# Kernel optimization log

Measured on AMD Instinct MI355X. Metric: run time of the kernel, lower is better.

Reference implementation:

```python
import jax, jax.numpy as jnp
import numpy as np

NUM_ENTS = 100000
NUM_RELS2 = 460  # num_rels * 2
H = 128
T = 4            # sequence_len snapshots
E = 200000       # edges per snapshot
SLOPE = (1.0 / 8.0 + 1.0 / 3.0) / 2.0  # F.rrelu in eval mode -> leaky with mean slope


def l2norm(x):
    # torch F.normalize(dim=1)
    n = jnp.linalg.norm(x, axis=-1, keepdims=True)
    return x / jnp.maximum(n, 1e-12)


def gru_cell(x, h, Wx, Wh, bx, bh):
    # torch.nn.GRUCell math
    gx = x @ Wx.T + bx  # [*, 3H]
    gh = h @ Wh.T + bh
    xr, xz, xn = jnp.split(gx, 3, axis=-1)
    hr, hz, hn = jnp.split(gh, 3, axis=-1)
    r = jax.nn.sigmoid(xr + hr)
    z = jax.nn.sigmoid(xz + hz)
    n = jnp.tanh(xn + r * hn)
    return (1.0 - z) * n + z * h


def rgcn_layer(h, rel, src, dst, etype, Wn, Wl):
    # UnionRGCNLayer (convgcn): msg = (h[src] + rel_emb[etype]) @ W_neighbor,
    # sum-aggregate to dst, normalize by in-degree, add self-loop transform, rrelu.
    msg = (h[src] + rel[etype]) @ Wn                        # [E, H]
    agg = jax.ops.segment_sum(msg, dst, num_segments=NUM_ENTS)
    deg = jax.ops.segment_sum(jnp.ones((msg.shape[0],), msg.dtype), dst,
                              num_segments=NUM_ENTS)
    agg = agg / jnp.maximum(deg, 1.0)[:, None]
    out = agg + h @ Wl                                      # self-loop
    return jnp.where(out >= 0, out, SLOPE * out)


def setup_inputs() -> dict:
    key = jax.random.key(0)
    ks = jax.random.split(key, 24)
    s = 0.05
    inp = {
        'src': jax.random.randint(ks[0], (T, E), 0, NUM_ENTS),
        'dst': jax.random.randint(ks[1], (T, E), 0, NUM_ENTS),
        'etype': jax.random.randint(ks[2], (T, E), 0, NUM_RELS2),
        'dynamic_emb': jax.random.normal(ks[3], (NUM_ENTS, H), jnp.float32),
        'emb_rel': jax.random.normal(ks[4], (NUM_RELS2, H), jnp.float32) * s,
        'Wn1': jax.random.normal(ks[5], (H, H), jnp.float32) * s,
        'Wl1': jax.random.normal(ks[6], (H, H), jnp.float32) * s,
        'Wn2': jax.random.normal(ks[7], (H, H), jnp.float32) * s,
        'Wl2': jax.random.normal(ks[8], (H, H), jnp.float32) * s,
        'gru_r_Wx': jax.random.normal(ks[9], (3 * H, 2 * H), jnp.float32) * s,
        'gru_r_Wh': jax.random.normal(ks[10], (3 * H, H), jnp.float32) * s,
        'gru_r_bx': jnp.zeros((3 * H,), jnp.float32),
        'gru_r_bh': jnp.zeros((3 * H,), jnp.float32),
        'gate_W': jax.random.normal(ks[11], (H, 2 * H), jnp.float32) * s,
        'gate_b': jnp.zeros((H,), jnp.float32),
        'tdiff_W': jax.random.normal(ks[12], (H, H), jnp.float32) * s,
        'tdiff_b': jnp.zeros((H,), jnp.float32),
        'time_gate_W': jax.random.normal(ks[13], (H, H), jnp.float32) * s,
        'time_gate_b': jnp.zeros((H,), jnp.float32),
    }
    return inp


def reference(src, dst, etype, dynamic_emb, emb_rel, Wn1, Wl1, Wn2, Wl2,
              gru_r_Wx, gru_r_Wh, gru_r_bx, gru_r_bh,
              gate_W, gate_b, tdiff_W, tdiff_b, time_gate_W, time_gate_b):
    h0 = l2norm(dynamic_emb)  # layer_norm=True path (F.normalize)

    def step(carry, g):
        h, rel = carry
        s, d, et = g
        # relation evolution via GRUCell(2H -> H)
        x_in = jnp.concatenate([emb_rel, rel], axis=1)
        rel_new = gru_cell(x_in, rel, gru_r_Wx, gru_r_Wh, gru_r_bx, gru_r_bh)
        # 2-layer RGCN message passing on snapshot graph
        cur = rgcn_layer(h, rel_new, s, d, et, Wn1, Wl1)
        cur = rgcn_layer(cur, rel_new, s, d, et, Wn2, Wl2)
        cur = l2norm(cur)
        # time gate
        tw = jax.nn.sigmoid(cur @ time_gate_W + time_gate_b)
        h_new = tw * cur + (1.0 - tw) * h
        # GatedFusion(current, prev)
        gate = jax.nn.sigmoid(jnp.concatenate([h_new, h], axis=1) @ gate_W.T + gate_b)
        h_new = gate * h_new + (1.0 - gate) * h
        # TemporalDifferenceFusion(current, prev)
        h_new = h_new + jax.nn.relu((h_new - h) @ tdiff_W.T + tdiff_b)
        return (h_new, rel_new), None

    (h, rel), _ = jax.lax.scan(step, (h0, emb_rel), (src, dst, etype))
    return h
```

## Files before the change

### kernel.cpp

```cpp
#include <hip/hip_runtime.h>
#include <hip/hip_bf16.h>

#define N_ENT 100000
#define HDIM 128
#define NE 200000
#define NR 460
#define NSTEP 4
#define SLOPE 0.22916666666666666f
#define NPAD 100352
#define SCAN_NB 98
#define HGRID 782

typedef __attribute__((ext_vector_type(8))) short short8;
typedef __attribute__((ext_vector_type(4))) float f32x4;

__device__ __forceinline__ float sigm(float x) { return 1.0f / (1.0f + __expf(-x)); }
__device__ __forceinline__ short f2bs(float f) {
    __hip_bfloat16 b = __float2bfloat16(f);
    short s; __builtin_memcpy(&s, &b, 2); return s;
}
__device__ __forceinline__ float bs2f(short s) {
    union { unsigned int u; float f; } c;
    c.u = ((unsigned int)(unsigned short)s) << 16;
    return c.f;
}

__global__ void zero_int_kernel(int* __restrict__ p, int n)
{
    int i = blockIdx.x * 256 + threadIdx.x;
    if (i < n) p[i] = 0;
}

__global__ void diag_kernel(float* o, float v)
{
    if (threadIdx.x == 0) o[0] = v;
}

__global__ __launch_bounds__(256)
void hist_gru_kernel(const int* __restrict__ dst, int* __restrict__ cnt,
                     float* rel, short* __restrict__ relb,
                     const float* __restrict__ emb_rel,
                     const float* __restrict__ WxT, const float* __restrict__ WhT,
                     const float* __restrict__ bx, const float* __restrict__ bh)
{
    if (blockIdx.x < HGRID) {
        int e = blockIdx.x * 256 + threadIdx.x;
        if (e < NE) atomicAdd(&cnt[dst[e]], 1);
        return;
    }
    __shared__ __align__(16) float x[256];
    __shared__ __align__(16) float hh[128];
    int b = blockIdx.x - HGRID;
    int j = threadIdx.x;
    float hj = 0.0f;
    if (j < 128) {
        hj = rel[b * HDIM + j];
        x[j] = emb_rel[b * HDIM + j];
        x[128 + j] = hj;
        hh[j] = hj;
    }
    __syncthreads();
    if (j >= 128) return;
    float xr = 0, xz = 0, xn = 0, hr = 0, hz = 0, hn = 0;
    for (int k = 0; k < 256; k++) {
        float xv = x[k];
        const float* w = &WxT[k * 384];
        xr += xv * w[j]; xz += xv * w[128 + j]; xn += xv * w[256 + j];
    }
    for (int k = 0; k < 128; k++) {
        float hv = hh[k];
        const float* w = &WhT[k * 384];
        hr += hv * w[j]; hz += hv * w[128 + j]; hn += hv * w[256 + j];
    }
    float r = sigm(xr + bx[j] + hr + bh[j]);
    float z = sigm(xz + bx[128 + j] + hz + bh[128 + j]);
    float n = tanhf(xn + bx[256 + j] + r * (hn + bh[256 + j]));
    float nv = (1.0f - z) * n + z * hj;
    rel[b * HDIM + j] = nv;
    relb[b * HDIM + j] = f2bs(nv);
}

__global__ __launch_bounds__(256)
void scan1_kernel(const int* __restrict__ cnt, int* __restrict__ rowptr,
                  int* __restrict__ bsum)
{
    __shared__ int ts[256];
    int b = blockIdx.x, t = threadIdx.x;
    int base = b * 1024 + t * 4;
    int4 v = *(const int4*)&cnt[base];
    int s = v.x + v.y + v.z + v.w;
    ts[t] = s;
    __syncthreads();
    for (int off = 1; off < 256; off <<= 1) {
        int x = 0;
        if (t >= off) x = ts[t - off];
        __syncthreads();
        if (t >= off) ts[t] += x;
        __syncthreads();
    }
    int excl = ts[t] - s;
    if (t == 255) bsum[b] = ts[t];
    rowptr[base + 0] = excl;
    rowptr[base + 1] = excl + v.x;
    rowptr[base + 2] = excl + v.x + v.y;
    rowptr[base + 3] = excl + v.x + v.y + v.z;
}

__global__ __launch_bounds__(128)
void scan2_kernel(int* __restrict__ bsum, int nb)
{
    __shared__ int ts[128];
    int t = threadIdx.x;
    int v = (t < nb) ? bsum[t] : 0;
    ts[t] = v;
    __syncthreads();
    for (int off = 1; off < 128; off <<= 1) {
        int x = 0;
        if (t >= off) x = ts[t - off];
        __syncthreads();
        if (t >= off) ts[t] += x;
        __syncthreads();
    }
    if (t < nb) bsum[t] = ts[t] - v;
}

__global__ void fill_kernel(const int* __restrict__ dst,
                            const int* __restrict__ rowptr,
                            const int* __restrict__ bsum,
                            int* __restrict__ cnt, int* __restrict__ eidx)
{
    int e = blockIdx.x * 256 + threadIdx.x;
    if (e < NE) {
        int d = dst[e];
        int p = atomicAdd(&cnt[d], -1);
        eidx[rowptr[d] + bsum[d >> 10] + p - 1] = e;
    }
}

__global__ void prep_kernel(
    const float* __restrict__ emb_rel,
    const float* __restrict__ Wx, const float* __restrict__ Wh,
    const float* __restrict__ Wn1, const float* __restrict__ Wl1,
    const float* __restrict__ Wn2, const float* __restrict__ Wl2,
    const float* __restrict__ tgW, const float* __restrict__ gateW,
    const float* __restrict__ tdW,
    float* __restrict__ rel,
    float* __restrict__ WxT, float* __restrict__ WhT,
    short* __restrict__ BT1, short* __restrict__ BT2,
    short* __restrict__ BTe1, short* __restrict__ BTe2,
    short* __restrict__ BTe3)
{
    int tid = blockIdx.x * blockDim.x + threadIdx.x;
    int nthr = gridDim.x * blockDim.x;
    for (int i = tid; i < NR * HDIM; i += nthr)
        rel[i] = emb_rel[i];
    for (int i = tid; i < 384 * 256; i += nthr) {
        int r = i >> 8, c = i & 255;
        WxT[c * 384 + r] = Wx[i];
    }
    for (int i = tid; i < 384 * 128; i += nthr) {
        int r = i >> 7, c = i & 127;
        WhT[c * 384 + r] = Wh[i];
    }
    for (int i = tid; i < 128 * 256; i += nthr) {
        int n = i >> 8, k = i & 255;
        float v1 = (k < 128) ? Wn1[k * 128 + n] : Wl1[(k - 128) * 128 + n];
        float v2 = (k < 128) ? Wn2[k * 128 + n] : Wl2[(k - 128) * 128 + n];
        BT1[n * 256 + k] = f2bs(v1);
        BT2[n * 256 + k] = f2bs(v2);
    }
    for (int i = tid; i < 128 * 128; i += nthr) {
        int n = i >> 7, k = i & 127;
        BTe1[n * 128 + k] = f2bs(tgW[k * 128 + n]);
        BTe3[n * 128 + k] = f2bs(tdW[n * 128 + k]);
    }
    for (int i = tid; i < 128 * 256; i += nthr) {
        int n = i >> 8, k = i & 255;
        BTe2[n * 256 + k] = f2bs(gateW[n * 256 + k]);
    }
}

__global__ __launch_bounds__(64)
void norm_init_kernel(const float* __restrict__ emb, short* __restrict__ hb)
{
    int row = blockIdx.x, lane = threadIdx.x;
    float v0 = emb[row * HDIM + lane];
    float v1 = emb[row * HDIM + 64 + lane];
    float s = v0 * v0 + v1 * v1;
    #pragma unroll
    for (int off = 32; off; off >>= 1) s += __shfl_xor(s, off);
    float invn = 1.0f / fmaxf(sqrtf(s), 1e-12f);
    hb[row * HDIM + lane] = f2bs(v0 * invn);
    hb[row * HDIM + 64 + lane] = f2bs(v1 * invn);
}

__global__ __launch_bounds__(256)
void gather_kernel(const int* __restrict__ src, const int* __restrict__ et,
                   const int* __restrict__ eidx, const int* __restrict__ rowptr,
                   const int* __restrict__ bsum,
                   const short* __restrict__ hb, const short* __restrict__ relb,
                   short* __restrict__ aggb, int lo, int hi)
{
    int idx = blockIdx.x * 256 + threadIdx.x;
    int r = lo + (idx >> 3);
    if (r >= hi) return;
    int c16 = (idx & 7) * 16;
    int p0 = rowptr[r] + bsum[r >> 10];
    int p1 = rowptr[r + 1] + bsum[(r + 1) >> 10];
    float v[16];
    #pragma unroll
    for (int j = 0; j < 16; j++) v[j] = 0.0f;

    int p = p0;
    for (; p + 2 <= p1; p += 2) {
        int e0 = eidx[p], e1 = eidx[p + 1];
        int s0 = src[e0], t0 = et[e0];
        int s1 = src[e1], t1 = et[e1];
        short8 h00 = *(const short8*)&hb[(long)s0 * HDIM + c16];
        short8 h01 = *(const short8*)&hb[(long)s0 * HDIM + c16 + 8];
        short8 h10 = *(const short8*)&hb[(long)s1 * HDIM + c16];
        short8 h11 = *(const short8*)&hb[(long)s1 * HDIM + c16 + 8];
        short8 r00 = *(const short8*)&relb[t0 * HDIM + c16];
        short8 r01 = *(const short8*)&relb[t0 * HDIM + c16 + 8];
        short8 r10 = *(const short8*)&relb[t1 * HDIM + c16];
        short8 r11 = *(const short8*)&relb[t1 * HDIM + c16 + 8];
        #pragma unroll
        for (int j = 0; j < 8; j++) {
            v[j]     += bs2f(h00[j]) + bs2f(r00[j]) + bs2f(h10[j]) + bs2f(r10[j]);
            v[8 + j] += bs2f(h01[j]) + bs2f(r01[j]) + bs2f(h11[j]) + bs2f(r11[j]);
        }
    }
    if (p < p1) {
        int e0 = eidx[p];
        int s0 = src[e0], t0 = et[e0];
        short8 h00 = *(const short8*)&hb[(long)s0 * HDIM + c16];
        short8 h01 = *(const short8*)&hb[(long)s0 * HDIM + c16 + 8];
        short8 r00 = *(const short8*)&relb[t0 * HDIM + c16];
        short8 r01 = *(const short8*)&relb[t0 * HDIM + c16 + 8];
        #pragma unroll
        for (int j = 0; j < 8; j++) {
            v[j]     += bs2f(h00[j]) + bs2f(r00[j]);
            v[8 + j] += bs2f(h01[j]) + bs2f(r01[j]);
        }
    }

    float rdeg = (p1 > p0) ? 1.0f / (float)(p1 - p0) : 0.0f;
    short8 o0, o1;
    #pragma unroll
    for (int j = 0; j < 8; j++) {
        o0[j] = f2bs(v[j] * rdeg);
        o1[j] = f2bs(v[8 + j] * rdeg);
    }
    *(short8*)&aggb[(long)(r - lo) * HDIM + c16] = o0;
    *(short8*)&aggb[(long)(r - lo) * HDIM + c16 + 8] = o1;
}

template<int F32OUT>
__global__ __launch_bounds__(256, 2)
void layer_gemm(const short* __restrict__ aggb, const short* __restrict__ hb,
                const short* __restrict__ BTg, float* __restrict__ outf,
                short* __restrict__ outb, int lo, int hi)
{
    __shared__ __align__(16) short smBT[128 * 256];
    const int tid = threadIdx.x;

    #pragma unroll
    for (int it = 0; it < 16; it++) {
        int s = it * 256 + tid;
        int row = s >> 5, k8 = s & 31;
        short8 v = *(const short8*)&BTg[row * 256 + k8 * 8];
        *(short8*)&smBT[row * 256 + 8 * (k8 ^ (row & 7))] = v;
    }
    __syncthreads();

    const int lane = tid & 63;
    const int wv = tid >> 6;
    const int m = lane & 15, q = lane >> 4;
    const int rowBase = lo + blockIdx.x * 256 + wv * 64;

    f32x4 acc[4][8];
    #pragma unroll
    for (int rt = 0; rt < 4; rt++)
        #pragma unroll
        for (int ct = 0; ct < 8; ct++)
            acc[rt][ct] = (f32x4)0.0f;

    for (int kc = 0; kc < 8; kc++) {
        short8 a[4];
        #pragma unroll
        for (int rt = 0; rt < 4; rt++) {
            int row = rowBase + rt * 16 + m;
            int k0 = kc * 32 + q * 8;
            if (row < hi) {
                if (kc < 4) {
                    a[rt] = *(const short8*)&aggb[(long)(row - lo) * HDIM + k0];
                } else {
                    a[rt] = *(const short8*)&hb[(long)row * HDIM + (k0 - 128)];
                }
            } else {
                short8 t;
                #pragma unroll
                for (int i = 0; i < 8; i++) t[i] = 0;
                a[rt] = t;
            }
        }
        short8 b[8];
        #pragma unroll
        for (int ct = 0; ct < 8; ct++)
            b[ct] = *(const short8*)&smBT[(ct * 16 + m) * 256
                                          + 8 * ((kc * 4 + q) ^ (m & 7))];
        #pragma unroll
        for (int rt = 0; rt < 4; rt++)
            #pragma unroll
            for (int ct = 0; ct < 8; ct++)
                acc[rt][ct] = __builtin_amdgcn_mfma_f32_16x16x32_bf16(
                    a[rt], b[ct], acc[rt][ct], 0, 0, 0);
    }

    #pragma unroll
    for (int rt = 0; rt < 4; rt++) {
        #pragma unroll
        for (int rg = 0; rg < 4; rg++) {
            int row = rowBase + rt * 16 + q * 4 + rg;
            if (row >= hi) continue;
            #pragma unroll
            for (int ct = 0; ct < 8; ct++) {
                int col = ct * 16 + m;
                float c = acc[rt][ct][rg];
                c = c >= 0.0f ? c : SLOPE * c;
                if (F32OUT) outf[(long)row * HDIM + col] = c;
                else        outb[(long)row * HDIM + col] = f2bs(c);
            }
        }
    }
}

#define ER 32
#define ES 136

__device__ __forceinline__ void stage_tile(
    const float* __restrict__ curf, const short* __restrict__ curb,
    const short* __restrict__ hb, long rb, int tid, int wf,
    short* cs, short* hd)
{
    #pragma unroll
    for (int it = 0; it < 2; it++) {
        int s = it * 256 + tid;
        int r = s >> 4, c8 = (s & 15) * 8;
        float x[8];
        if (wf) {
            const float* pc = &curf[(rb + r) * HDIM + c8];
            float4 c0 = *(const float4*)pc, c1 = *(const float4*)(pc + 4);
            x[0]=c0.x; x[1]=c0.y; x[2]=c0.z; x[3]=c0.w;
            x[4]=c1.x; x[5]=c1.y; x[6]=c1.z; x[7]=c1.w;
        } else {
            short8 cv = *(const short8*)&curb[(rb + r) * HDIM + c8];
            #pragma unroll
            for (int j = 0; j < 8; j++) x[j] = bs2f(cv[j]);
        }
        short8 th = *(const short8*)&hb[(rb + r) * HDIM + c8];
        float ss = x[0]*x[0] + x[1]*x[1] + x[2]*x[2] + x[3]*x[3]
                 + x[4]*x[4] + x[5]*x[5] + x[6]*x[6] + x[7]*x[7];
        ss += __shfl_xor(ss, 1);
        ss += __shfl_xor(ss, 2);
        ss += __shfl_xor(ss, 4);
        ss += __shfl_xor(ss, 8);
        float inv = 1.0f / fmaxf(sqrtf(ss), 1e-12f);
        short8 tc;
        #pragma unroll
        for (int j = 0; j < 8; j++) tc[j] = f2bs(x[j] * inv);
        *(short8*)&cs[r * ES + c8] = tc;
        *(short8*)&hd[r * ES + c8] = th;
    }
}

__device__ __forceinline__ void mm128_d(const short* As0, const short* As1,
                                        const short* __restrict__ Bg,
                                        int wr0, int ct0, int m, int q,
                                        f32x4 a0[4], f32x4 a1[4])
{
    #pragma unroll
    for (int ct = 0; ct < 4; ct++) { a0[ct] = (f32x4)0.0f; a1[ct] = (f32x4)0.0f; }
    #pragma unroll
    for (int kc = 0; kc < 4; kc++) {
        int k0 = kc * 32 + q * 8;
        short8 av0 = *(const short8*)&As0[(wr0 + m) * ES + k0];
        short8 av1 = *(const short8*)&As1[(wr0 + m) * ES + k0];
        #pragma unroll
        for (int ct = 0; ct < 4; ct++) {
            short8 b = *(const short8*)&Bg[((ct0 + ct) * 16 + m) * 128 + k0];
            a0[ct] = __builtin_amdgcn_mfma_f32_16x16x32_bf16(av0, b, a0[ct], 0, 0, 0);
            a1[ct] = __builtin_amdgcn_mfma_f32_16x16x32_bf16(av1, b, a1[ct], 0, 0, 0);
        }
    }
}

__device__ __forceinline__ void mm256_d(const short* cs0, const short* hd0,
                                        const short* cs1, const short* hd1,
                                        const short* __restrict__ Bg,
                                        int wr0, int ct0, int m, int q,
                                        f32x4 a0[4], f32x4 a1[4])
{
    #pragma unroll
    for (int ct = 0; ct < 4; ct++) { a0[ct] = (f32x4)0.0f; a1[ct] = (f32x4)0.0f; }
    #pragma unroll
    for (int kc = 0; kc < 8; kc++) {
        int k0 = kc * 32 + q * 8;
        short8 av0 = (kc < 4) ? *(const short8*)&cs0[(wr0 + m) * ES + k0]
                              : *(const short8*)&hd0[(wr0 + m) * ES + (k0 - 128)];
        short8 av1 = (kc < 4) ? *(const short8*)&cs1[(wr0 + m) * ES + k0]
                              : *(const short8*)&hd1[(wr0 + m) * ES + (k0 - 128)];
        #pragma unroll
        for (int ct = 0; ct < 4; ct++) {
            short8 b = *(const short8*)&Bg[((ct0 + ct) * 16 + m) * 256 + k0];
            a0[ct] = __builtin_amdgcn_mfma_f32_16x16x32_bf16(av0, b, a0[ct], 0, 0, 0);
            a1[ct] = __builtin_amdgcn_mfma_f32_16x16x32_bf16(av1, b, a1[ct], 0, 0, 0);
        }
    }
}

__device__ __forceinline__ void epi1_f(const f32x4 acc[4], const float btr[4],
                                       short* cs, const short* hd,
                                       int wr0, int ct0, int m, int q)
{
    #pragma unroll
    for (int ct = 0; ct < 4; ct++) {
        int col = (ct0 + ct) * 16 + m;
        #pragma unroll
        for (int rg = 0; rg < 4; rg++) {
            int rl = wr0 + q * 4 + rg;
            float tw = sigm(acc[ct][rg] + btr[ct]);
            float curn = bs2f(cs[rl * ES + col]);
            float hv = bs2f(hd[rl * ES + col]);
            cs[rl * ES + col] = f2bs(tw * curn + (1.0f - tw) * hv);
        }
    }
}

__device__ __forceinline__ void epi2_f(const f32x4 acc[4], const float bgr[4],
                                       short* cs, short* hd,
                                       int wr0, int ct0, int m, int q)
{
    #pragma unroll
    for (int ct = 0; ct < 4; ct++) {
        int col = (ct0 + ct) * 16 + m;
        #pragma unroll
        for (int rg = 0; rg < 4; rg++) {
            int rl = wr0 + q * 4 + rg;
            float g = sigm(acc[ct][rg] + bgr[ct]);
            float h1v = bs2f(cs[rl * ES + col]);
            float hv = bs2f(hd[rl * ES + col]);
            float h2 = g * h1v + (1.0f - g) * hv;
            cs[rl * ES + col] = f2bs(h2);
            hd[rl * ES + col] = f2bs(h2 - hv);
        }
    }
}

__device__ __forceinline__ void fin_f(const f32x4 acc[4], const float btdr[4],
                                      short* cs, long rb,
                                      float* __restrict__ outp, int wf,
                                      int wr0, int ct0, int m, int q)
{
    #pragma unroll
    for (int ct = 0; ct < 4; ct++) {
        int col = (ct0 + ct) * 16 + m;
        #pragma unroll
        for (int rg = 0; rg < 4; rg++) {
            int rl = wr0 + q * 4 + rg;
            float td = fmaxf(acc[ct][rg] + btdr[ct], 0.0f);
            float val = bs2f(cs[rl * ES + col]) + td;
            if (wf) outp[(rb + rl) * HDIM + col] = val;
            else    cs[rl * ES + col] = f2bs(val);
        }
    }
}

__global__ __launch_bounds__(256, 4)
void fused_epi_kernel(const float* __restrict__ curf, const short* __restrict__ curb,
                      const short* __restrict__ hb,
                      const short* __restrict__ BTe1, const short* __restrict__ BTe2,
                      const short* __restrict__ BTe3,
                      const float* __restrict__ bt, const float* __restrict__ bg,
                      const float* __restrict__ btd,
                      float* __restrict__ outp, short* __restrict__ abfo, int wf)
{
    __shared__ __align__(16) short cs[2][ER * ES];
    __shared__ __align__(16) short hd[2][ER * ES];
    const int tid = threadIdx.x;
    const long row0 = (long)blockIdx.x * (2 * ER);
    const long row1 = row0 + ER;
    const bool t1v = (row1 < N_ENT);

    stage_tile(curf, curb, hb, row0, tid, wf, cs[0], hd[0]);
    if (t1v) stage_tile(curf, curb, hb, row1, tid, wf, cs[1], hd[1]);
    __syncthreads();

    const int wv = tid >> 6, lane = tid & 63;
    const int m = lane & 15, q = lane >> 4;
    const int wr0 = (wv >> 1) * 16;
    const int ct0 = (wv & 1) * 4;

    float btr[4], bgr[4], btdr[4];
    #pragma unroll
    for (int ct = 0; ct < 4; ct++) {
        btr[ct]  = bt[(ct0 + ct) * 16 + m];
        bgr[ct]  = bg[(ct0 + ct) * 16 + m];
        btdr[ct] = btd[(ct0 + ct) * 16 + m];
    }

    f32x4 a0[4], a1[4];

    mm128_d(cs[0], cs[1], BTe1, wr0, ct0, m, q, a0, a1);
    __syncthreads();
    epi1_f(a0, btr, cs[0], hd[0], wr0, ct0, m, q);
    epi1_f(a1, btr, cs[1], hd[1], wr0, ct0, m, q);
    __syncthreads();

    mm256_d(cs[0], hd[0], cs[1], hd[1], BTe2, wr0, ct0, m, q, a0, a1);
    __syncthreads();
    epi2_f(a0, bgr, cs[0], hd[0], wr0, ct0, m, q);
    epi2_f(a1, bgr, cs[1], hd[1], wr0, ct0, m, q);
    __syncthreads();

    mm128_d(hd[0], hd[1], BTe3, wr0, ct0, m, q, a0, a1);
    fin_f(a0, btdr, cs[0], row0, outp, wf, wr0, ct0, m, q);
    if (t1v) fin_f(a1, btdr, cs[1], row1, outp, wf, wr0, ct0, m, q);

    if (!wf) {
        __syncthreads();
        #pragma unroll
        for (int it = 0; it < 4; it++) {
            int slot = it * 256 + tid;
            int tile = slot >> 9;
            int rr = (slot >> 4) & 31;
            int c8 = (slot & 15) * 8;
            if (tile == 0 || t1v) {
                long gr = row0 + tile * ER + rr;
                *(short8*)&abfo[gr * HDIM + c8] =
                    *(const short8*)&cs[tile][rr * ES + c8];
            }
        }
    }
}

extern "C" void kernel_launch(void* const* d_in, const int* in_sizes, int n_in,
                              void* d_out, int out_size, void* d_ws, size_t ws_size,
                              hipStream_t stream)
{
    const int* src = (const int*)d_in[0];
    const int* dst = (const int*)d_in[1];
    const int* ety = (const int*)d_in[2];
    const float* dyn     = (const float*)d_in[3];
    const float* emb_rel = (const float*)d_in[4];
    const float* Wn1     = (const float*)d_in[5];
    const float* Wl1     = (const float*)d_in[6];
    const float* Wn2     = (const float*)d_in[7];
    const float* Wl2     = (const float*)d_in[8];
    const float* gWx     = (const float*)d_in[9];
    const float* gWh     = (const float*)d_in[10];
    const float* gbx     = (const float*)d_in[11];
    const float* gbh     = (const float*)d_in[12];
    const float* gateW   = (const float*)d_in[13];
    const float* gateb   = (const float*)d_in[14];
    const float* tdW     = (const float*)d_in[15];
    const float* tdb     = (const float*)d_in[16];
    const float* tgW     = (const float*)d_in[17];
    const float* tgb     = (const float*)d_in[18];

    const long NH = (long)N_ENT * HDIM;
    float* ws = (float*)d_ws;
    long off = 0;
    short* Abf  = (short*)(ws + off); off += NH / 2;
    short* Bb   = (short*)(ws + off); off += NH / 2;
    short* Cb   = (short*)(ws + off); off += NH / 2;
    float* rel  = ws + off; off += (long)NR * HDIM;
    short* relb = (short*)(ws + off); off += (NR * HDIM) / 2;
    float* WxT  = ws + off; off += 98304;
    float* WhT  = ws + off; off += 49152;
    short* BT1  = (short*)(ws + off); off += 16384;
    short* BT2  = (short*)(ws + off); off += 16384;
    short* BTe1 = (short*)(ws + off); off += 8192;
    short* BTe2 = (short*)(ws + off); off += 16384;
    short* BTe3 = (short*)(ws + off); off += 8192;
    int* rowptr = (int*)(ws + off); off += NPAD;
    int* cnt    = (int*)(ws + off); off += NPAD;
    int* eidx   = (int*)(ws + off); off += 200704;
    int* bsum   = (int*)(ws + off); off += 128;
    short* aggb = (short*)(ws + off);
    float* C    = (float*)d_out;

    const long avail = (long)(ws_size / 4) - off;
    const int cand[5] = {100000, 50000, 25008, 12512, 6256};
    int chunk = -1;
    for (int c = 0; c < 5; c++)
        if (avail >= (long)cand[c] * 64) { chunk = cand[c]; break; }

    if (chunk < 0) {
        diag_kernel<<<1, 64, 0, stream>>>((float*)d_out, (float)ws_size);
        return;
    }

    prep_kernel<<<256, 256, 0, stream>>>(
        emb_rel, gWx, gWh, Wn1, Wl1, Wn2, Wl2, tgW, gateW, tdW,
        rel, WxT, WhT, BT1, BT2, BTe1, BTe2, BTe3);

    norm_init_kernel<<<N_ENT, 64, 0, stream>>>(dyn, Abf);

    zero_int_kernel<<<(NPAD + 255) / 256, 256, 0, stream>>>(cnt, NPAD);

    const int egrid = (NE + 255) / 256;
    const int fe_grid = (N_ENT + 63) / 64;

    for (int t = 0; t < NSTEP; t++) {
        const int* st = src + (long)t * NE;
        const int* dt = dst + (long)t * NE;
        const int* et = ety + (long)t * NE;

        hist_gru_kernel<<<HGRID + NR, 256, 0, stream>>>(
            dt, cnt, rel, relb, emb_rel, WxT, WhT, gbx, gbh);
        scan1_kernel<<<SCAN_NB, 256, 0, stream>>>(cnt, rowptr, bsum);
        scan2_kernel<<<1, 128, 0, stream>>>(bsum, SCAN_NB);
        fill_kernel<<<egrid, 256, 0, stream>>>(dt, rowptr, bsum, cnt, eidx);

        int wf = (t == NSTEP - 1) ? 1 : 0;

        for (int lo = 0; lo < N_ENT; lo += chunk) {
            int hi = lo + chunk > N_ENT ? N_ENT : lo + chunk;
            gather_kernel<<<((hi - lo) * 8 + 255) / 256, 256, 0, stream>>>(
                st, et, eidx, rowptr, bsum, Abf, relb, aggb, lo, hi);
            layer_gemm<0><<<(hi - lo + 255) / 256, 256, 0, stream>>>(
                aggb, Abf, BT1, nullptr, Bb, lo, hi);
        }
        for (int lo = 0; lo < N_ENT; lo += chunk) {
            int hi = lo + chunk > N_ENT ? N_ENT : lo + chunk;
            gather_kernel<<<((hi - lo) * 8 + 255) / 256, 256, 0, stream>>>(
                st, et, eidx, rowptr, bsum, Bb, relb, aggb, lo, hi);
            if (wf)
                layer_gemm<1><<<(hi - lo + 255) / 256, 256, 0, stream>>>(
                    aggb, Bb, BT2, C, nullptr, lo, hi);
            else
                layer_gemm<0><<<(hi - lo + 255) / 256, 256, 0, stream>>>(
                    aggb, Bb, BT2, nullptr, Cb, lo, hi);
        }

        fused_epi_kernel<<<fe_grid, 256, 0, stream>>>(
            C, Cb, Abf, BTe1, BTe2, BTe3, tgb, gateb, tdb, C, Abf, wf);
    }
}
```

Measured before the change: 908.6 us.

## Batch CSR build for all snapshots upfront and fold GRU into epilogue kernel

Builds the destination-sorted edge index (histogram, scan, fill) for all four snapshots at once using 2D grids before the time loop, instead of four per-step kernels inside it. The relation GRU for the next step is merged into the tail blocks of the fused epilogue kernel, with a standalone GRU kernel only for the first step. This cuts per-step launches and serial dependencies. The cost is four times the CSR workspace and extra branching in the epilogue kernel.

```diff
diff --git a/kernel.cpp b/kernel.cpp
--- a/kernel.cpp
+++ b/kernel.cpp
@@ -9,7 +9,9 @@
 #define SLOPE 0.22916666666666666f
 #define NPAD 100352
 #define SCAN_NB 98
-#define HGRID 782
+#define EGRID 782
+#define ESZ 200704
+#define FEG 1563
 
 typedef __attribute__((ext_vector_type(8))) short short8;
 typedef __attribute__((ext_vector_type(4))) float f32x4;
@@ -36,104 +38,71 @@
     if (threadIdx.x == 0) o[0] = v;
 }
 
+__global__ void hist4_kernel(const int* __restrict__ dst, int* __restrict__ cnt4)
+{
+    int t = blockIdx.y;
+    int e = blockIdx.x * 256 + threadIdx.x;
+    if (e < NE) atomicAdd(&cnt4[t * NPAD + dst[(long)t * NE + e]], 1);
+}
+
 __global__ __launch_bounds__(256)
-void hist_gru_kernel(const int* __restrict__ dst, int* __restrict__ cnt,
-                     float* rel, short* __restrict__ relb,
-                     const float* __restrict__ emb_rel,
-                     const float* __restrict__ WxT, const float* __restrict__ WhT,
-                     const float* __restrict__ bx, const float* __restrict__ bh)
-{
-    if (blockIdx.x < HGRID) {
-        int e = blockIdx.x * 256 + threadIdx.x;
-        if (e < NE) atomicAdd(&cnt[dst[e]], 1);
-        return;
-    }
-    __shared__ __align__(16) float x[256];
-    __shared__ __align__(16) float hh[128];
-    int b = blockIdx.x - HGRID;
-    int j = threadIdx.x;
-    float hj = 0.0f;
-    if (j < 128) {
-        hj = rel[b * HDIM + j];
-        x[j] = emb_rel[b * HDIM + j];
-        x[128 + j] = hj;
-        hh[j] = hj;
-    }
-    __syncthreads();
-    if (j >= 128) return;
-    float xr = 0, xz = 0, xn = 0, hr = 0, hz = 0, hn = 0;
-    for (int k = 0; k < 256; k++) {
-        float xv = x[k];
-        const float* w = &WxT[k * 384];
-        xr += xv * w[j]; xz += xv * w[128 + j]; xn += xv * w[256 + j];
-    }
-    for (int k = 0; k < 128; k++) {
-        float hv = hh[k];
-        const float* w = &WhT[k * 384];
-        hr += hv * w[j]; hz += hv * w[128 + j]; hn += hv * w[256 + j];
-    }
-    float r = sigm(xr + bx[j] + hr + bh[j]);
-    float z = sigm(xz + bx[128 + j] + hz + bh[128 + j]);
-    float n = tanhf(xn + bx[256 + j] + r * (hn + bh[256 + j]));
-    float nv = (1.0f - z) * n + z * hj;
-    rel[b * HDIM + j] = nv;
-    relb[b * HDIM + j] = f2bs(nv);
-}
-
-__global__ __launch_bounds__(256)
-void scan1_kernel(const int* __restrict__ cnt, int* __restrict__ rowptr,
-                  int* __restrict__ bsum)
+void scan1_4_kernel(const int* __restrict__ cnt4, int* __restrict__ rowptr4,
+                    int* __restrict__ bsum4)
 {
     __shared__ int ts[256];
-    int b = blockIdx.x, t = threadIdx.x;
-    int base = b * 1024 + t * 4;
-    int4 v = *(const int4*)&cnt[base];
+    int t = blockIdx.y;
+    int b = blockIdx.x, tt = threadIdx.x;
+    int base = t * NPAD + b * 1024 + tt * 4;
+    int4 v = *(const int4*)&cnt4[base];
     int s = v.x + v.y + v.z + v.w;
-    ts[t] = s;
+    ts[tt] = s;
     __syncthreads();
     for (int off = 1; off < 256; off <<= 1) {
         int x = 0;
-        if (t >= off) x = ts[t - off];
+        if (tt >= off) x = ts[tt - off];
         __syncthreads();
-        if (t >= off) ts[t] += x;
+        if (tt >= off) ts[tt] += x;
         __syncthreads();
     }
-    int excl = ts[t] - s;
-    if (t == 255) bsum[b] = ts[t];
-    rowptr[base + 0] = excl;
-    rowptr[base + 1] = excl + v.x;
-    rowptr[base + 2] = excl + v.x + v.y;
-    rowptr[base + 3] = excl + v.x + v.y + v.z;
+    int excl = ts[tt] - s;
+    if (tt == 255) bsum4[t * 128 + b] = ts[tt];
+    rowptr4[base + 0] = excl;
+    rowptr4[base + 1] = excl + v.x;
+    rowptr4[base + 2] = excl + v.x + v.y;
+    rowptr4[base + 3] = excl + v.x + v.y + v.z;
 }
 
 __global__ __launch_bounds__(128)
-void scan2_kernel(int* __restrict__ bsum, int nb)
+void scan2_4_kernel(int* __restrict__ bsum4)
 {
     __shared__ int ts[128];
-    int t = threadIdx.x;
-    int v = (t < nb) ? bsum[t] : 0;
-    ts[t] = v;
+    int t = blockIdx.x;
+    int tt = threadIdx.x;
+    int v = (tt < SCAN_NB) ? bsum4[t * 128 + tt] : 0;
+    ts[tt] = v;
     __syncthreads();
     for (int off = 1; off < 128; off <<= 1) {
         int x = 0;
-        if (t >= off) x = ts[t - off];
+        if (tt >= off) x = ts[tt - off];
         __syncthreads();
-        if (t >= off) ts[t] += x;
+        if (tt >= off) ts[tt] += x;
         __syncthreads();
     }
-    if (t < nb) bsum[t] = ts[t] - v;
-}
-
-__global__ void fill_kernel(const int* __restrict__ dst,
-                            const int* __restrict__ rowptr,
-                            const int* __restrict__ bsum,
-                            int* __restrict__ cnt, int* __restrict__ eidx)
-{
+    if (tt < SCAN_NB) bsum4[t * 128 + tt] = ts[tt] - v;
+}
+
+__global__ void fill4_kernel(const int* __restrict__ dst,
+                             const int* __restrict__ rowptr4,
+                             const int* __restrict__ bsum4,
+                             int* __restrict__ cnt4, int* __restrict__ eidx4)
+{
+    int t = blockIdx.y;
     int e = blockIdx.x * 256 + threadIdx.x;
     if (e < NE) {
-        int d = dst[e];
-        int p = atomicAdd(&cnt[d], -1);
-        eidx[rowptr[d] + bsum[d >> 10] + p - 1] = e;
+        int d = dst[(long)t * NE + e];
+        int p = atomicAdd(&cnt4[t * NPAD + d], -1);
+        eidx4[(long)t * ESZ + rowptr4[t * NPAD + d]
+              + bsum4[t * 128 + (d >> 10)] + p - 1] = e;
     }
 }
 
@@ -192,6 +161,39 @@
     float invn = 1.0f / fmaxf(sqrtf(s), 1e-12f);
     hb[row * HDIM + lane] = f2bs(v0 * invn);
     hb[row * HDIM + 64 + lane] = f2bs(v1 * invn);
+}
+
+__global__ __launch_bounds__(128)
+void gru_kernel(float* rel, short* __restrict__ relb,
+                const float* __restrict__ emb_rel,
+                const float* __restrict__ WxT, const float* __restrict__ WhT,
+                const float* __restrict__ bx, const float* __restrict__ bh)
+{
+    __shared__ __align__(16) float x[256];
+    __shared__ __align__(16) float hh[128];
+    int b = blockIdx.x, j = threadIdx.x;
+    float hj = rel[b * HDIM + j];
+    x[j] = emb_rel[b * HDIM + j];
+    x[128 + j] = hj;
+    hh[j] = hj;
+    __syncthreads();
+    float xr = 0, xz = 0, xn = 0, hr = 0, hz = 0, hn = 0;
+    for (int k = 0; k < 256; k++) {
+        float xv = x[k];
+        const float* w = &WxT[k * 384];
+        xr += xv * w[j]; xz += xv * w[128 + j]; xn += xv * w[256 + j];
+    }
+    for (int k = 0; k < 128; k++) {
+        float hv = hh[k];
+        const float* w = &WhT[k * 384];
+        hr += hv * w[j]; hz += hv * w[128 + j]; hn += hv * w[256 + j];
+    }
+    float r = sigm(xr + bx[j] + hr + bh[j]);
+    float z = sigm(xz + bx[128 + j] + hz + bh[128 + j]);
+    float n = tanhf(xn + bx[256 + j] + r * (hn + bh[256 + j]));
+    float nv = (1.0f - z) * n + z * hj;
+    rel[b * HDIM + j] = nv;
+    relb[b * HDIM + j] = f2bs(nv);
 }
 
 __global__ __launch_bounds__(256)
@@ -483,11 +485,50 @@
                       const short* __restrict__ BTe3,
                       const float* __restrict__ bt, const float* __restrict__ bg,
                       const float* __restrict__ btd,
-                      float* __restrict__ outp, short* __restrict__ abfo, int wf)
+                      float* __restrict__ outp, short* __restrict__ abfo, int wf,
+                      float* rel, short* __restrict__ relb,
+                      const float* __restrict__ emb_rel,
+                      const float* __restrict__ WxT, const float* __restrict__ WhT,
+                      const float* __restrict__ gbx, const float* __restrict__ gbh)
 {
     __shared__ __align__(16) short cs[2][ER * ES];
     __shared__ __align__(16) short hd[2][ER * ES];
     const int tid = threadIdx.x;
+
+    if (blockIdx.x >= FEG) {
+        float* x = (float*)cs;
+        float* hh = x + 256;
+        int b = blockIdx.x - FEG;
+        int j = tid;
+        float hj = 0.0f;
+        if (j < 128) {
+            hj = rel[b * HDIM + j];
+            x[j] = emb_rel[b * HDIM + j];
+            x[128 + j] = hj;
+            hh[j] = hj;
+        }
+        __syncthreads();
+        if (j >= 128) return;
+        float xr = 0, xz = 0, xn = 0, hr = 0, hz = 0, hn = 0;
+        for (int k = 0; k < 256; k++) {
+            float xv = x[k];
+            const float* w = &WxT[k * 384];
+            xr += xv * w[j]; xz += xv * w[128 + j]; xn += xv * w[256 + j];
+        }
+        for (int k = 0; k < 128; k++) {
+            float hv = hh[k];
+            const float* w = &WhT[k * 384];
+            hr += hv * w[j]; hz += hv * w[128 + j]; hn += hv * w[256 + j];
+        }
+        float r = sigm(xr + gbx[j] + hr + gbh[j]);
+        float z = sigm(xz + gbx[128 + j] + hz + gbh[128 + j]);
+        float n = tanhf(xn + gbx[256 + j] + r * (hn + gbh[256 + j]));
+        float nv = (1.0f - z) * n + z * hj;
+        rel[b * HDIM + j] = nv;
+        relb[b * HDIM + j] = f2bs(nv);
+        return;
+    }
+
     const long row0 = (long)blockIdx.x * (2 * ER);
     const long row1 = row0 + ER;
     const bool t1v = (row1 < N_ENT);
@@ -583,10 +624,10 @@
     short* BTe1 = (short*)(ws + off); off += 8192;
     short* BTe2 = (short*)(ws + off); off += 16384;
     short* BTe3 = (short*)(ws + off); off += 8192;
-    int* rowptr = (int*)(ws + off); off += NPAD;
-    int* cnt    = (int*)(ws + off); off += NPAD;
-    int* eidx   = (int*)(ws + off); off += 200704;
-    int* bsum   = (int*)(ws + off); off += 128;
+    int* rowptr4 = (int*)(ws + off); off += 4 * NPAD;
+    int* cnt4    = (int*)(ws + off); off += 4 * NPAD;
+    int* eidx4   = (int*)(ws + off); off += 4 * ESZ;
+    int* bsum4   = (int*)(ws + off); off += 4 * 128;
     short* aggb = (short*)(ws + off);
     float* C    = (float*)d_out;
 
@@ -607,35 +648,37 @@
 
     norm_init_kernel<<<N_ENT, 64, 0, stream>>>(dyn, Abf);
 
-    zero_int_kernel<<<(NPAD + 255) / 256, 256, 0, stream>>>(cnt, NPAD);
-
-    const int egrid = (NE + 255) / 256;
-    const int fe_grid = (N_ENT + 63) / 64;
+    zero_int_kernel<<<(4 * NPAD + 255) / 256, 256, 0, stream>>>(cnt4, 4 * NPAD);
+    {
+        dim3 g2(EGRID, 4), g3(SCAN_NB, 4);
+        hist4_kernel<<<g2, 256, 0, stream>>>(dst, cnt4);
+        scan1_4_kernel<<<g3, 256, 0, stream>>>(cnt4, rowptr4, bsum4);
+        scan2_4_kernel<<<4, 128, 0, stream>>>(bsum4);
+        fill4_kernel<<<g2, 256, 0, stream>>>(dst, rowptr4, bsum4, cnt4, eidx4);
+    }
+
+    gru_kernel<<<NR, 128, 0, stream>>>(rel, relb, emb_rel, WxT, WhT, gbx, gbh);
 
     for (int t = 0; t < NSTEP; t++) {
         const int* st = src + (long)t * NE;
-        const int* dt = dst + (long)t * NE;
         const int* et = ety + (long)t * NE;
-
-        hist_gru_kernel<<<HGRID + NR, 256, 0, stream>>>(
-            dt, cnt, rel, relb, emb_rel, WxT, WhT, gbx, gbh);
-        scan1_kernel<<<SCAN_NB, 256, 0, stream>>>(cnt, rowptr, bsum);
-        scan2_kernel<<<1, 128, 0, stream>>>(bsum, SCAN_NB);
-        fill_kernel<<<egrid, 256, 0, stream>>>(dt, rowptr, bsum, cnt, eidx);
+        const int* rp = rowptr4 + t * NPAD;
+        const int* bs = bsum4 + t * 128;
+        const int* ei = eidx4 + (long)t * ESZ;
 
         int wf = (t == NSTEP - 1) ? 1 : 0;
 
         for (int lo = 0; lo < N_ENT; lo += chunk) {
             int hi = lo + chunk > N_ENT ? N_ENT : lo + chunk;
             gather_kernel<<<((hi - lo) * 8 + 255) / 256, 256, 0, stream>>>(
-                st, et, eidx, rowptr, bsum, Abf, relb, aggb, lo, hi);
+                st, et, ei, rp, bs, Abf, relb, aggb, lo, hi);
             layer_gemm<0><<<(hi - lo + 255) / 256, 256, 0, stream>>>(
                 aggb, Abf, BT1, nullptr, Bb, lo, hi);
         }
         for (int lo = 0; lo < N_ENT; lo += chunk) {
             int hi = lo + chunk > N_ENT ? N_ENT : lo + chunk;
             gather_kernel<<<((hi - lo) * 8 + 255) / 256, 256, 0, stream>>>(
-                st, et, eidx, rowptr, bsum, Bb, relb, aggb, lo, hi);
+                st, et, ei, rp, bs, Bb, relb, aggb, lo, hi);
             if (wf)
                 layer_gemm<1><<<(hi - lo + 255) / 256, 256, 0, stream>>>(
                     aggb, Bb, BT2, C, nullptr, lo, hi);
@@ -644,7 +687,9 @@
                     aggb, Bb, BT2, nullptr, Cb, lo, hi);
         }
 
-        fused_epi_kernel<<<fe_grid, 256, 0, stream>>>(
-            C, Cb, Abf, BTe1, BTe2, BTe3, tgb, gateb, tdb, C, Abf, wf);
-    }
-}
+        int ngru = wf ? 0 : NR;
+        fused_epi_kernel<<<FEG + ngru, 256, 0, stream>>>(
+            C, Cb, Abf, BTe1, BTe2, BTe3, tgb, gateb, tdb, C, Abf, wf,
+            rel, relb, emb_rel, WxT, WhT, gbx, gbh);
+    }
+}
```

After: 833.0 us. 8.3% less time.
